# Optimization experiments

Hardware: AMD Instinct MI355X
Metric: run time of the kernel (lower is better)

Reference implementation:

```python
import jax, jax.numpy as jnp
import numpy as np

N_NODES = 100000


def gcn_conv(x, W, b, row, col, ew, n_nodes):
    """PyG GCNConv: add self-loops (weight 1), symmetric normalization,
    out[c] = sum_{(r,c) in E} norm * (x @ W)[r] + b."""
    sl = jnp.arange(n_nodes, dtype=row.dtype)
    row2 = jnp.concatenate([row, sl])
    col2 = jnp.concatenate([col, sl])
    ew2 = jnp.concatenate([ew, jnp.ones((n_nodes,), dtype=ew.dtype)])
    deg = jax.ops.segment_sum(ew2, col2, num_segments=n_nodes)  # [N]
    dinv = jnp.where(deg > 0, jax.lax.rsqrt(jnp.where(deg > 0, deg, 1.0)), 0.0)
    norm = dinv[row2] * ew2 * dinv[col2]                         # [E+N]
    h = x @ W                                                    # [N, out]
    msg = h[row2] * norm[:, None]                                # gather + scale
    out = jax.ops.segment_sum(msg, col2, num_segments=n_nodes)   # scatter-add
    return out + b


def setup_inputs() -> dict:
    key = jax.random.key(0)
    k1, k2, k3, k4, k5 = jax.random.split(key, 5)
    F_IN, HID, C = 512, 16, 40
    E = 3200000
    x = jax.random.normal(k1, (N_NODES, F_IN), dtype=jnp.float32)
    edge_index = jax.random.randint(k2, (2, E), 0, N_NODES, dtype=jnp.int64)
    edge_weight = jax.random.uniform(k3, (E,), dtype=jnp.float32)
    # Glorot-ish init for weights
    W1 = jax.random.normal(k4, (F_IN, HID), dtype=jnp.float32) / np.sqrt(F_IN)
    b1 = jnp.zeros((HID,), dtype=jnp.float32)
    W2 = jax.random.normal(k5, (HID, C), dtype=jnp.float32) / np.sqrt(HID)
    b2 = jnp.zeros((C,), dtype=jnp.float32)
    return {"x": x, "edge_index": edge_index, "edge_weight": edge_weight,
            "W1": W1, "b1": b1, "W2": W2, "b2": b2}


def reference(x, edge_index, edge_weight, W1, b1, W2, b2):
    row, col = edge_index[0], edge_index[1]
    h = jax.nn.relu(gcn_conv(x, W1, b1, row, col, edge_weight, N_NODES))
    # dropout p=0.1 is identity at inference; DFALayer/DFA are identity in forward
    logits = gcn_conv(h, W2, b2, row, col, edge_weight, N_NODES)
    return jax.nn.log_softmax(logits, axis=1)
```

## Files before the change

kernel.cpp:

```cpp
#include <hip/hip_runtime.h>
#include <hip/hip_bf16.h>
#include <math.h>

#define F_IN 512
#define HID  16
#define C_OUT 40

#define BSH    7
#define BNODES 128
#define MAXNB  1024

#define EPB 8192
#define CTH 512

__device__ __forceinline__ unsigned short f2bf(float f) {
    unsigned u = __float_as_uint(f);
    unsigned r = (u + 0x7FFF + ((u >> 16) & 1)) >> 16;
    return (unsigned short)r;
}
__device__ __forceinline__ float bf2f(unsigned short h) {
    return __uint_as_float(((unsigned)h) << 16);
}

__global__ __launch_bounds__(1024) void k_zero(int* __restrict__ g, int n) {
    int t = threadIdx.x;
    if (t < n) g[t] = 0;
}

__global__ __launch_bounds__(CTH) void k_count(const int* __restrict__ col,
                                               int* __restrict__ gcnt,
                                               int E, int NB) {
    __shared__ int lc[MAXNB];
    int t = threadIdx.x;
    for (int i = t; i < NB; i += CTH) lc[i] = 0;
    __syncthreads();
    int base = blockIdx.x * EPB;
#pragma unroll
    for (int i = 0; i < EPB / CTH; ++i) {
        int e = base + t + i * CTH;
        if (e < E) atomicAdd(&lc[col[e] >> BSH], 1);
    }
    __syncthreads();
    for (int i = t; i < NB; i += CTH)
        if (lc[i]) atomicAdd(&gcnt[i], lc[i]);
}

__global__ __launch_bounds__(1024) void k_scan(const int* __restrict__ gcnt,
                                               int* __restrict__ bo,
                                               int* __restrict__ bcur,
                                               int* __restrict__ offs,
                                               int NB, int N, int E) {
    __shared__ int s[1024];
    int t = threadIdx.x;
    int v = (t < NB) ? gcnt[t] : 0;
    s[t] = v;
    __syncthreads();
    for (int off = 1; off < 1024; off <<= 1) {
        int x = (t >= off) ? s[t - off] : 0;
        __syncthreads();
        s[t] += x;
        __syncthreads();
    }
    if (t < NB) { int o = s[t] - v; bo[t] = o; bcur[t] = o; }
    if (t == 0) { bo[NB] = E; offs[N] = E; }
}

__global__ __launch_bounds__(CTH) void k_part(const int* __restrict__ row,
                                              const int* __restrict__ col,
                                              const float* __restrict__ ew,
                                              int* __restrict__ bcur,
                                              int2* __restrict__ st,
                                              int E, int NB) {
    __shared__ int lc[MAXNB];
    __shared__ int lb[MAXNB];
    int t = threadIdx.x;
    for (int i = t; i < NB; i += CTH) lc[i] = 0;
    __syncthreads();
    int base = blockIdx.x * EPB;
#pragma unroll
    for (int i = 0; i < EPB / CTH; ++i) {
        int e = base + t + i * CTH;
        if (e < E) atomicAdd(&lc[col[e] >> BSH], 1);
    }
    __syncthreads();
    for (int i = t; i < NB; i += CTH) {
        int c = lc[i];
        lb[i] = c ? atomicAdd(&bcur[i], c) : 0;
    }
    __syncthreads();
    for (int i = t; i < NB; i += CTH) lc[i] = 0;
    __syncthreads();
#pragma unroll
    for (int i = 0; i < EPB / CTH; ++i) {
        int e = base + t + i * CTH;
        if (e < E) {
            int c = col[e];
            int b = c >> BSH;
            int r = atomicAdd(&lc[b], 1);
            st[lb[b] + r] = make_int2((row[e] << BSH) | (c & (BNODES - 1)),
                                      __float_as_int(ew[e]));
        }
    }
}

__global__ __launch_bounds__(256) void k_sort(const int* __restrict__ bo,
                                              const int2* __restrict__ st,
                                              int2* __restrict__ st2,
                                              int* __restrict__ offs,
                                              float* __restrict__ dinv, int N) {
    __shared__ int cnt[BNODES];
    __shared__ float wsum[BNODES];
    __shared__ int off[BNODES];
    int t = threadIdx.x;
    int b = blockIdx.x;
    if (t < BNODES) { cnt[t] = 0; wsum[t] = 0.0f; }
    __syncthreads();
    int beg = bo[b], end = bo[b + 1];
    for (int e = beg + t; e < end; e += 256) {
        int2 rec = st[e];
        int cl = rec.x & (BNODES - 1);
        atomicAdd(&cnt[cl], 1);
        atomicAdd(&wsum[cl], __int_as_float(rec.y));
    }
    __syncthreads();
    if (t < BNODES) off[t] = cnt[t];
    __syncthreads();
    for (int o = 1; o < BNODES; o <<= 1) {
        int v = (t < BNODES && t >= o) ? off[t - o] : 0;
        __syncthreads();
        if (t < BNODES) off[t] += v;
        __syncthreads();
    }
    if (t < BNODES) {
        int ex = off[t] - cnt[t];
        off[t] = ex;
        int n = b * BNODES + t;
        if (n < N) {
            offs[n] = beg + ex;
            dinv[n] = rsqrtf(1.0f + wsum[t]);
        }
        cnt[t] = 0;
    }
    __syncthreads();
    for (int e = beg + t; e < end; e += 256) {
        int2 rec = st[e];
        int cl = rec.x & (BNODES - 1);
        int r = atomicAdd(&cnt[cl], 1);
        st2[beg + off[cl] + r] = make_int2(rec.x >> BSH, rec.y);
    }
}

#define ROWS_PER_WAVE 16

__global__ __launch_bounds__(256, 1) void k_gemm1(const float* __restrict__ x,
                                                  const float* __restrict__ W,
                                                  const float* __restrict__ dinv,
                                                  unsigned short* __restrict__ hb,
                                                  int N) {
    const int t = threadIdx.x;
    const int lane = t & 63;
    const int wv = blockIdx.x * 4 + (t >> 6);
    const int r0 = wv * ROWS_PER_WAVE;
    if (r0 >= N) return;
    const int rend = (r0 + ROWS_PER_WAVE < N) ? r0 + ROWS_PER_WAVE : N;

    float4 Wa[4][4], Wb[4][4];
    const float4* W4 = (const float4*)W;
#pragma unroll
    for (int q = 0; q < 4; ++q)
#pragma unroll
        for (int j4 = 0; j4 < 4; ++j4) {
            Wa[q][j4] = W4[(4 * lane + q) * 4 + j4];
            Wb[q][j4] = W4[(256 + 4 * lane + q) * 4 + j4];
        }

    const float4* xb4 = (const float4*)x;
    float4 pa = xb4[(size_t)r0 * 128 + lane];
    float4 pb = xb4[(size_t)r0 * 128 + 64 + lane];

    for (int r = r0; r < rend; ++r) {
        float4 ca = pa, cb = pb;
        if (r + 1 < rend) {
            pa = xb4[(size_t)(r + 1) * 128 + lane];
            pb = xb4[(size_t)(r + 1) * 128 + 64 + lane];
        }
        float acc[16];
#pragma unroll
        for (int j = 0; j < 16; ++j) acc[j] = 0.0f;
        const float xs0[4] = {ca.x, ca.y, ca.z, ca.w};
        const float xs1[4] = {cb.x, cb.y, cb.z, cb.w};
#pragma unroll
        for (int q = 0; q < 4; ++q) {
#pragma unroll
            for (int j4 = 0; j4 < 4; ++j4) {
                acc[j4 * 4 + 0] += xs0[q] * Wa[q][j4].x;
                acc[j4 * 4 + 1] += xs0[q] * Wa[q][j4].y;
                acc[j4 * 4 + 2] += xs0[q] * Wa[q][j4].z;
                acc[j4 * 4 + 3] += xs0[q] * Wa[q][j4].w;
            }
        }
#pragma unroll
        for (int q = 0; q < 4; ++q) {
#pragma unroll
            for (int j4 = 0; j4 < 4; ++j4) {
                acc[j4 * 4 + 0] += xs1[q] * Wb[q][j4].x;
                acc[j4 * 4 + 1] += xs1[q] * Wb[q][j4].y;
                acc[j4 * 4 + 2] += xs1[q] * Wb[q][j4].z;
                acc[j4 * 4 + 3] += xs1[q] * Wb[q][j4].w;
            }
        }

        const int b0 = lane & 1;
        float v8[8];
#pragma unroll
        for (int m = 0; m < 8; ++m) {
            float lo = acc[m], hi = acc[m + 8];
            float sent = b0 ? lo : hi;
            float recv = __shfl_xor(sent, 1, 64);
            float keep = b0 ? hi : lo;
            v8[m] = keep + recv;
        }
        const int b1 = (lane >> 1) & 1;
        float v4[4];
#pragma unroll
        for (int m = 0; m < 4; ++m) {
            float lo = v8[m], hi = v8[m + 4];
            float sent = b1 ? lo : hi;
            float recv = __shfl_xor(sent, 2, 64);
            float keep = b1 ? hi : lo;
            v4[m] = keep + recv;
        }
        const int b2 = (lane >> 2) & 1;
        float v2[2];
#pragma unroll
        for (int m = 0; m < 2; ++m) {
            float lo = v4[m], hi = v4[m + 2];
            float sent = b2 ? lo : hi;
            float recv = __shfl_xor(sent, 4, 64);
            float keep = b2 ? hi : lo;
            v2[m] = keep + recv;
        }
        const int b3 = (lane >> 3) & 1;
        float v1;
        {
            float lo = v2[0], hi = v2[1];
            float sent = b3 ? lo : hi;
            float recv = __shfl_xor(sent, 8, 64);
            float keep = b3 ? hi : lo;
            v1 = keep + recv;
        }
        v1 += __shfl_xor(v1, 16, 64);
        v1 += __shfl_xor(v1, 32, 64);

        float d = dinv[r];
        if (lane < 16) {
            int j = ((lane & 1) << 3) | (((lane >> 1) & 1) << 2) |
                    (((lane >> 2) & 1) << 1) | ((lane >> 3) & 1);
            hb[(size_t)r * HID + j] = f2bf(d * v1);
        }
    }
}

__global__ __launch_bounds__(256) void k_agg1(const int* __restrict__ offs,
                                              const int2* __restrict__ st2,
                                              const float* __restrict__ dinv,
                                              const unsigned short* __restrict__ srcb,
                                              const float* __restrict__ bias,
                                              unsigned short* __restrict__ dstb,
                                              int N) {
    int t = threadIdx.x;
    int lane = t & 63, w = t >> 6;
    int n = blockIdx.x * 4 + w;
    if (n >= N) return;
    int q = lane & 3, i = lane >> 2;
    int beg = offs[n], end = offs[n + 1];
    float4 acc = make_float4(0.f, 0.f, 0.f, 0.f);
    for (int e = beg + i; e < end; e += 16) {
        int2 rec = st2[e];
        float wt = __int_as_float(rec.y);
        ushort4 v = ((const ushort4*)(srcb + (size_t)rec.x * HID))[q];
        acc.x += wt * bf2f(v.x);
        acc.y += wt * bf2f(v.y);
        acc.z += wt * bf2f(v.z);
        acc.w += wt * bf2f(v.w);
    }
#pragma unroll
    for (int off = 4; off < 64; off <<= 1) {
        acc.x += __shfl_xor(acc.x, off, 64);
        acc.y += __shfl_xor(acc.y, off, 64);
        acc.z += __shfl_xor(acc.z, off, 64);
        acc.w += __shfl_xor(acc.w, off, 64);
    }
    if (i == 0) {
        float d = dinv[n];
        ushort4 sv = ((const ushort4*)(srcb + (size_t)n * HID))[q];
        float4 bq = ((const float4*)bias)[q];
        float r0 = d * fmaxf(d * (acc.x + bf2f(sv.x)) + bq.x, 0.f);
        float r1 = d * fmaxf(d * (acc.y + bf2f(sv.y)) + bq.y, 0.f);
        float r2 = d * fmaxf(d * (acc.z + bf2f(sv.z)) + bq.z, 0.f);
        float r3 = d * fmaxf(d * (acc.w + bf2f(sv.w)) + bq.w, 0.f);
        ((ushort4*)(dstb + (size_t)n * HID))[q] =
            make_ushort4(f2bf(r0), f2bf(r1), f2bf(r2), f2bf(r3));
    }
}

__global__ __launch_bounds__(256) void k_agg2(const int* __restrict__ offs,
                                              const int2* __restrict__ st2,
                                              const float* __restrict__ dinv,
                                              const unsigned short* __restrict__ srcb,
                                              const float* __restrict__ W2,
                                              const float* __restrict__ b2,
                                              float* __restrict__ out, int N) {
    __shared__ float Ws[HID * C_OUT];
    __shared__ float bs[C_OUT];
    int t = threadIdx.x;
    for (int iw = t; iw < HID * C_OUT; iw += 256) Ws[iw] = W2[iw];
    if (t < C_OUT) bs[t] = b2[t];
    __syncthreads();

    int lane = t & 63, w = t >> 6;
    int n = blockIdx.x * 4 + w;
    if (n >= N) return;
    int q = lane & 3, i = lane >> 2;
    int beg = offs[n], end = offs[n + 1];
    float4 acc = make_float4(0.f, 0.f, 0.f, 0.f);
    for (int e = beg + i; e < end; e += 16) {
        int2 rec = st2[e];
        float wt = __int_as_float(rec.y);
        ushort4 v = ((const ushort4*)(srcb + (size_t)rec.x * HID))[q];
        acc.x += wt * bf2f(v.x);
        acc.y += wt * bf2f(v.y);
        acc.z += wt * bf2f(v.z);
        acc.w += wt * bf2f(v.w);
    }
#pragma unroll
    for (int off = 4; off < 64; off <<= 1) {
        acc.x += __shfl_xor(acc.x, off, 64);
        acc.y += __shfl_xor(acc.y, off, 64);
        acc.z += __shfl_xor(acc.z, off, 64);
        acc.w += __shfl_xor(acc.w, off, 64);
    }
    float d = dinv[n];
    ushort4 sv = ((const ushort4*)(srcb + (size_t)n * HID))[q];
    float gq[4];
    gq[0] = d * (acc.x + bf2f(sv.x));
    gq[1] = d * (acc.y + bf2f(sv.y));
    gq[2] = d * (acc.z + bf2f(sv.z));
    gq[3] = d * (acc.w + bf2f(sv.w));
    float g16[16];
    int base = lane & ~3;
#pragma unroll
    for (int qq = 0; qq < 4; ++qq) {
#pragma unroll
        for (int k = 0; k < 4; ++k)
            g16[qq * 4 + k] = __shfl(gq[k], base + qq, 64);
    }
    float logit = -INFINITY;
    if (lane < C_OUT) {
        float a = bs[lane];
#pragma unroll
        for (int j = 0; j < HID; ++j) a += g16[j] * Ws[j * C_OUT + lane];
        logit = a;
    }
    float m = logit;
#pragma unroll
    for (int off = 32; off > 0; off >>= 1) m = fmaxf(m, __shfl_xor(m, off, 64));
    float ex = (lane < C_OUT) ? __expf(logit - m) : 0.0f;
    float s = ex;
#pragma unroll
    for (int off = 32; off > 0; off >>= 1) s += __shfl_xor(s, off, 64);
    if (lane < C_OUT) out[(size_t)n * C_OUT + lane] = logit - m - __logf(s);
}

extern "C" void kernel_launch(void* const* d_in, const int* in_sizes, int n_in,
                              void* d_out, int out_size, void* d_ws, size_t ws_size,
                              hipStream_t stream) {
    const float* x   = (const float*)d_in[0];
    const int*   ei  = (const int*)d_in[1];
    const float* ew  = (const float*)d_in[2];
    const float* W1  = (const float*)d_in[3];
    const float* b1  = (const float*)d_in[4];
    const float* W2  = (const float*)d_in[5];
    const float* b2  = (const float*)d_in[6];
    float* out = (float*)d_out;

    const int N = in_sizes[0] / F_IN;
    const int E = in_sizes[2];
    const int* row = ei;
    const int* col = ei + E;
    const int NB = (N + BNODES - 1) >> BSH;

    int* wsi = (int*)d_ws;
    size_t o = 0;
    int* gcnt  = wsi + o; o += MAXNB;
    int* bo    = wsi + o; o += MAXNB + 1;
    int* bcur  = wsi + o; o += MAXNB;
    int* offs  = wsi + o; o += (size_t)N + 8;
    float* dinv = (float*)(wsi + o); o += N;
    unsigned short* h1b = (unsigned short*)(wsi + o); o += (size_t)N * HID / 2;
    unsigned short* a1b = (unsigned short*)(wsi + o); o += (size_t)N * HID / 2;
    int2* st   = (int2*)(wsi + o); o += (size_t)E * 2;
    int2* st2  = (int2*)(wsi + o); o += (size_t)E * 2;

    int gC = (E + EPB - 1) / EPB;
    int gW = (N + 3) / 4;
    int gG = (N + 4 * ROWS_PER_WAVE - 1) / (4 * ROWS_PER_WAVE);

    k_zero<<<1, 1024, 0, stream>>>(gcnt, NB);
    k_count<<<gC, CTH, 0, stream>>>(col, gcnt, E, NB);
    k_scan<<<1, 1024, 0, stream>>>(gcnt, bo, bcur, offs, NB, N, E);
    k_part<<<gC, CTH, 0, stream>>>(row, col, ew, bcur, st, E, NB);
    k_sort<<<NB, 256, 0, stream>>>(bo, st, st2, offs, dinv, N);
    k_gemm1<<<gG, 256, 0, stream>>>(x, W1, dinv, h1b, N);
    k_agg1<<<gW, 256, 0, stream>>>(offs, st2, dinv, h1b, b1, a1b, N);
    k_agg2<<<gW, 256, 0, stream>>>(offs, st2, dinv, a1b, W2, b2, out, N);
}
```

Baseline: 594.2 us.

## Drop per-node sort; aggregate bucketed edges via shared-memory atomics per block

Removes the second-level counting sort (k_sort) and CSR offsets. Degree and aggregation now run straight on the bucket-partitioned edge list: each 512-thread block owns a 128-node bucket and scatter-adds weighted neighbor features into a padded shared-memory accumulator, with a one-step software prefetch of the next record. agg2 is restructured so 4 threads per node each compute 10 logits. This saves one full pass over the edge array (read and write of st2) at the cost of LDS float atomics and contention on hot nodes, and it makes accumulation order nondeterministic.

```diff
diff --git a/kernel.cpp b/kernel.cpp
--- a/kernel.cpp
+++ b/kernel.cpp
@@ -12,6 +12,8 @@
 
 #define EPB 8192
 #define CTH 512
+#define ATH 512
+#define APAD 17
 
 __device__ __forceinline__ unsigned short f2bf(float f) {
     unsigned u = __float_as_uint(f);
@@ -48,8 +50,7 @@
 __global__ __launch_bounds__(1024) void k_scan(const int* __restrict__ gcnt,
                                                int* __restrict__ bo,
                                                int* __restrict__ bcur,
-                                               int* __restrict__ offs,
-                                               int NB, int N, int E) {
+                                               int NB, int E) {
     __shared__ int s[1024];
     int t = threadIdx.x;
     int v = (t < NB) ? gcnt[t] : 0;
@@ -62,7 +63,7 @@
         __syncthreads();
     }
     if (t < NB) { int o = s[t] - v; bo[t] = o; bcur[t] = o; }
-    if (t == 0) { bo[NB] = E; offs[N] = E; }
+    if (t == 0) bo[NB] = E;
 }
 
 __global__ __launch_bounds__(CTH) void k_part(const int* __restrict__ row,
@@ -103,50 +104,22 @@
     }
 }
 
-__global__ __launch_bounds__(256) void k_sort(const int* __restrict__ bo,
-                                              const int2* __restrict__ st,
-                                              int2* __restrict__ st2,
-                                              int* __restrict__ offs,
-                                              float* __restrict__ dinv, int N) {
-    __shared__ int cnt[BNODES];
+__global__ __launch_bounds__(ATH) void k_deg(const int* __restrict__ bo,
+                                             const int2* __restrict__ st,
+                                             float* __restrict__ dinv, int N) {
     __shared__ float wsum[BNODES];
-    __shared__ int off[BNODES];
-    int t = threadIdx.x;
-    int b = blockIdx.x;
-    if (t < BNODES) { cnt[t] = 0; wsum[t] = 0.0f; }
+    int t = threadIdx.x, b = blockIdx.x;
+    if (t < BNODES) wsum[t] = 0.0f;
     __syncthreads();
     int beg = bo[b], end = bo[b + 1];
-    for (int e = beg + t; e < end; e += 256) {
+    for (int e = beg + t; e < end; e += ATH) {
         int2 rec = st[e];
-        int cl = rec.x & (BNODES - 1);
-        atomicAdd(&cnt[cl], 1);
-        atomicAdd(&wsum[cl], __int_as_float(rec.y));
-    }
-    __syncthreads();
-    if (t < BNODES) off[t] = cnt[t];
-    __syncthreads();
-    for (int o = 1; o < BNODES; o <<= 1) {
-        int v = (t < BNODES && t >= o) ? off[t - o] : 0;
-        __syncthreads();
-        if (t < BNODES) off[t] += v;
-        __syncthreads();
-    }
+        atomicAdd(&wsum[rec.x & (BNODES - 1)], __int_as_float(rec.y));
+    }
+    __syncthreads();
     if (t < BNODES) {
-        int ex = off[t] - cnt[t];
-        off[t] = ex;
         int n = b * BNODES + t;
-        if (n < N) {
-            offs[n] = beg + ex;
-            dinv[n] = rsqrtf(1.0f + wsum[t]);
-        }
-        cnt[t] = 0;
-    }
-    __syncthreads();
-    for (int e = beg + t; e < end; e += 256) {
-        int2 rec = st[e];
-        int cl = rec.x & (BNODES - 1);
-        int r = atomicAdd(&cnt[cl], 1);
-        st2[beg + off[cl] + r] = make_int2(rec.x >> BSH, rec.y);
+        if (n < N) dinv[n] = rsqrtf(1.0f + wsum[t]);
     }
 }
 
@@ -261,115 +234,145 @@
     }
 }
 
-__global__ __launch_bounds__(256) void k_agg1(const int* __restrict__ offs,
-                                              const int2* __restrict__ st2,
+__global__ __launch_bounds__(ATH) void k_agg1(const int* __restrict__ bo,
+                                              const int2* __restrict__ st,
                                               const float* __restrict__ dinv,
                                               const unsigned short* __restrict__ srcb,
                                               const float* __restrict__ bias,
                                               unsigned short* __restrict__ dstb,
                                               int N) {
-    int t = threadIdx.x;
-    int lane = t & 63, w = t >> 6;
-    int n = blockIdx.x * 4 + w;
-    if (n >= N) return;
-    int q = lane & 3, i = lane >> 2;
-    int beg = offs[n], end = offs[n + 1];
-    float4 acc = make_float4(0.f, 0.f, 0.f, 0.f);
-    for (int e = beg + i; e < end; e += 16) {
-        int2 rec = st2[e];
-        float wt = __int_as_float(rec.y);
-        ushort4 v = ((const ushort4*)(srcb + (size_t)rec.x * HID))[q];
-        acc.x += wt * bf2f(v.x);
-        acc.y += wt * bf2f(v.y);
-        acc.z += wt * bf2f(v.z);
-        acc.w += wt * bf2f(v.w);
-    }
-#pragma unroll
-    for (int off = 4; off < 64; off <<= 1) {
-        acc.x += __shfl_xor(acc.x, off, 64);
-        acc.y += __shfl_xor(acc.y, off, 64);
-        acc.z += __shfl_xor(acc.z, off, 64);
-        acc.w += __shfl_xor(acc.w, off, 64);
-    }
-    if (i == 0) {
+    __shared__ float acc[BNODES * APAD];
+    int t = threadIdx.x, b = blockIdx.x;
+    for (int i = t; i < BNODES * APAD; i += ATH) acc[i] = 0.0f;
+    __syncthreads();
+
+    int beg = bo[b], end = bo[b + 1];
+    const int q = t & 3;
+    int e0 = beg + (t >> 2);
+    int2 r0 = make_int2(0, 0);
+    float4 v0 = make_float4(0.f, 0.f, 0.f, 0.f);
+    if (e0 < end) {
+        r0 = st[e0];
+        ushort4 u = ((const ushort4*)(srcb + (size_t)(r0.x >> BSH) * HID))[q];
+        v0 = make_float4(bf2f(u.x), bf2f(u.y), bf2f(u.z), bf2f(u.w));
+    }
+    while (e0 < end) {
+        int e1 = e0 + (ATH / 4);
+        int2 r1 = r0;
+        float4 v1 = v0;
+        if (e1 < end) {
+            r1 = st[e1];
+            ushort4 u = ((const ushort4*)(srcb + (size_t)(r1.x >> BSH) * HID))[q];
+            v1 = make_float4(bf2f(u.x), bf2f(u.y), bf2f(u.z), bf2f(u.w));
+        }
+        float wt = __int_as_float(r0.y);
+        float* a = &acc[(r0.x & (BNODES - 1)) * APAD + q * 4];
+        atomicAdd(a + 0, wt * v0.x);
+        atomicAdd(a + 1, wt * v0.y);
+        atomicAdd(a + 2, wt * v0.z);
+        atomicAdd(a + 3, wt * v0.w);
+        e0 = e1; r0 = r1; v0 = v1;
+    }
+    __syncthreads();
+
+    int nl = t >> 2;
+    int n = b * BNODES + nl;
+    if (n < N) {
         float d = dinv[n];
         ushort4 sv = ((const ushort4*)(srcb + (size_t)n * HID))[q];
         float4 bq = ((const float4*)bias)[q];
-        float r0 = d * fmaxf(d * (acc.x + bf2f(sv.x)) + bq.x, 0.f);
-        float r1 = d * fmaxf(d * (acc.y + bf2f(sv.y)) + bq.y, 0.f);
-        float r2 = d * fmaxf(d * (acc.z + bf2f(sv.z)) + bq.z, 0.f);
-        float r3 = d * fmaxf(d * (acc.w + bf2f(sv.w)) + bq.w, 0.f);
+        const float* a = &acc[nl * APAD + q * 4];
+        float o0 = d * fmaxf(d * (a[0] + bf2f(sv.x)) + bq.x, 0.f);
+        float o1 = d * fmaxf(d * (a[1] + bf2f(sv.y)) + bq.y, 0.f);
+        float o2 = d * fmaxf(d * (a[2] + bf2f(sv.z)) + bq.z, 0.f);
+        float o3 = d * fmaxf(d * (a[3] + bf2f(sv.w)) + bq.w, 0.f);
         ((ushort4*)(dstb + (size_t)n * HID))[q] =
-            make_ushort4(f2bf(r0), f2bf(r1), f2bf(r2), f2bf(r3));
-    }
-}
-
-__global__ __launch_bounds__(256) void k_agg2(const int* __restrict__ offs,
-                                              const int2* __restrict__ st2,
+            make_ushort4(f2bf(o0), f2bf(o1), f2bf(o2), f2bf(o3));
+    }
+}
+
+__global__ __launch_bounds__(ATH) void k_agg2(const int* __restrict__ bo,
+                                              const int2* __restrict__ st,
                                               const float* __restrict__ dinv,
                                               const unsigned short* __restrict__ srcb,
                                               const float* __restrict__ W2,
                                               const float* __restrict__ b2,
                                               float* __restrict__ out, int N) {
+    __shared__ float acc[BNODES * APAD];
     __shared__ float Ws[HID * C_OUT];
     __shared__ float bs[C_OUT];
-    int t = threadIdx.x;
-    for (int iw = t; iw < HID * C_OUT; iw += 256) Ws[iw] = W2[iw];
+    int t = threadIdx.x, b = blockIdx.x;
+    for (int i = t; i < BNODES * APAD; i += ATH) acc[i] = 0.0f;
+    for (int i = t; i < HID * C_OUT; i += ATH) Ws[i] = W2[i];
     if (t < C_OUT) bs[t] = b2[t];
     __syncthreads();
 
-    int lane = t & 63, w = t >> 6;
-    int n = blockIdx.x * 4 + w;
+    int beg = bo[b], end = bo[b + 1];
+    const int q = t & 3;
+    int e0 = beg + (t >> 2);
+    int2 r0 = make_int2(0, 0);
+    float4 v0 = make_float4(0.f, 0.f, 0.f, 0.f);
+    if (e0 < end) {
+        r0 = st[e0];
+        ushort4 u = ((const ushort4*)(srcb + (size_t)(r0.x >> BSH) * HID))[q];
+        v0 = make_float4(bf2f(u.x), bf2f(u.y), bf2f(u.z), bf2f(u.w));
+    }
+    while (e0 < end) {
+        int e1 = e0 + (ATH / 4);
+        int2 r1 = r0;
+        float4 v1 = v0;
+        if (e1 < end) {
+            r1 = st[e1];
+            ushort4 u = ((const ushort4*)(srcb + (size_t)(r1.x >> BSH) * HID))[q];
+            v1 = make_float4(bf2f(u.x), bf2f(u.y), bf2f(u.z), bf2f(u.w));
+        }
+        float wt = __int_as_float(r0.y);
+        float* a = &acc[(r0.x & (BNODES - 1)) * APAD + q * 4];
+        atomicAdd(a + 0, wt * v0.x);
+        atomicAdd(a + 1, wt * v0.y);
+        atomicAdd(a + 2, wt * v0.z);
+        atomicAdd(a + 3, wt * v0.w);
+        e0 = e1; r0 = r1; v0 = v1;
+    }
+    __syncthreads();
+
+    int nl = t >> 2;
+    int n = b * BNODES + nl;
     if (n >= N) return;
-    int q = lane & 3, i = lane >> 2;
-    int beg = offs[n], end = offs[n + 1];
-    float4 acc = make_float4(0.f, 0.f, 0.f, 0.f);
-    for (int e = beg + i; e < end; e += 16) {
-        int2 rec = st2[e];
-        float wt = __int_as_float(rec.y);
-        ushort4 v = ((const ushort4*)(srcb + (size_t)rec.x * HID))[q];
-        acc.x += wt * bf2f(v.x);
-        acc.y += wt * bf2f(v.y);
-        acc.z += wt * bf2f(v.z);
-        acc.w += wt * bf2f(v.w);
-    }
-#pragma unroll
-    for (int off = 4; off < 64; off <<= 1) {
-        acc.x += __shfl_xor(acc.x, off, 64);
-        acc.y += __shfl_xor(acc.y, off, 64);
-        acc.z += __shfl_xor(acc.z, off, 64);
-        acc.w += __shfl_xor(acc.w, off, 64);
-    }
     float d = dinv[n];
-    ushort4 sv = ((const ushort4*)(srcb + (size_t)n * HID))[q];
-    float gq[4];
-    gq[0] = d * (acc.x + bf2f(sv.x));
-    gq[1] = d * (acc.y + bf2f(sv.y));
-    gq[2] = d * (acc.z + bf2f(sv.z));
-    gq[3] = d * (acc.w + bf2f(sv.w));
     float g16[16];
-    int base = lane & ~3;
-#pragma unroll
-    for (int qq = 0; qq < 4; ++qq) {
-#pragma unroll
-        for (int k = 0; k < 4; ++k)
-            g16[qq * 4 + k] = __shfl(gq[k], base + qq, 64);
-    }
-    float logit = -INFINITY;
-    if (lane < C_OUT) {
-        float a = bs[lane];
-#pragma unroll
-        for (int j = 0; j < HID; ++j) a += g16[j] * Ws[j * C_OUT + lane];
-        logit = a;
-    }
-    float m = logit;
-#pragma unroll
-    for (int off = 32; off > 0; off >>= 1) m = fmaxf(m, __shfl_xor(m, off, 64));
-    float ex = (lane < C_OUT) ? __expf(logit - m) : 0.0f;
-    float s = ex;
-#pragma unroll
-    for (int off = 32; off > 0; off >>= 1) s += __shfl_xor(s, off, 64);
-    if (lane < C_OUT) out[(size_t)n * C_OUT + lane] = logit - m - __logf(s);
+    const ushort4* sp = (const ushort4*)(srcb + (size_t)n * HID);
+#pragma unroll
+    for (int p = 0; p < 4; ++p) {
+        ushort4 sv = sp[p];
+        const float* a = &acc[nl * APAD + p * 4];
+        g16[p * 4 + 0] = d * (a[0] + bf2f(sv.x));
+        g16[p * 4 + 1] = d * (a[1] + bf2f(sv.y));
+        g16[p * 4 + 2] = d * (a[2] + bf2f(sv.z));
+        g16[p * 4 + 3] = d * (a[3] + bf2f(sv.w));
+    }
+    const int cb = q * 10;
+    float lg[10];
+    float m = -INFINITY;
+#pragma unroll
+    for (int c = 0; c < 10; ++c) {
+        float a = bs[cb + c];
+#pragma unroll
+        for (int j = 0; j < HID; ++j) a += g16[j] * Ws[j * C_OUT + cb + c];
+        lg[c] = a;
+        m = fmaxf(m, a);
+    }
+    m = fmaxf(m, __shfl_xor(m, 1, 64));
+    m = fmaxf(m, __shfl_xor(m, 2, 64));
+    float s = 0.0f;
+#pragma unroll
+    for (int c = 0; c < 10; ++c) s += __expf(lg[c] - m);
+    s += __shfl_xor(s, 1, 64);
+    s += __shfl_xor(s, 2, 64);
+    float ls = __logf(s);
+    float* op = out + (size_t)n * C_OUT + cb;
+#pragma unroll
+    for (int c = 0; c < 10; ++c) op[c] = lg[c] - m - ls;
 }
 
 extern "C" void kernel_launch(void* const* d_in, const int* in_sizes, int n_in,
@@ -395,23 +398,20 @@
     int* gcnt  = wsi + o; o += MAXNB;
     int* bo    = wsi + o; o += MAXNB + 1;
     int* bcur  = wsi + o; o += MAXNB;
-    int* offs  = wsi + o; o += (size_t)N + 8;
     float* dinv = (float*)(wsi + o); o += N;
     unsigned short* h1b = (unsigned short*)(wsi + o); o += (size_t)N * HID / 2;
     unsigned short* a1b = (unsigned short*)(wsi + o); o += (size_t)N * HID / 2;
     int2* st   = (int2*)(wsi + o); o += (size_t)E * 2;
-    int2* st2  = (int2*)(wsi + o); o += (size_t)E * 2;
 
     int gC = (E + EPB - 1) / EPB;
-    int gW = (N + 3) / 4;
     int gG = (N + 4 * ROWS_PER_WAVE - 1) / (4 * ROWS_PER_WAVE);
 
     k_zero<<<1, 1024, 0, stream>>>(gcnt, NB);
     k_count<<<gC, CTH, 0, stream>>>(col, gcnt, E, NB);
-    k_scan<<<1, 1024, 0, stream>>>(gcnt, bo, bcur, offs, NB, N, E);
+    k_scan<<<1, 1024, 0, stream>>>(gcnt, bo, bcur, NB, E);
     k_part<<<gC, CTH, 0, stream>>>(row, col, ew, bcur, st, E, NB);
-    k_sort<<<NB, 256, 0, stream>>>(bo, st, st2, offs, dinv, N);
+    k_deg<<<NB, ATH, 0, stream>>>(bo, st, dinv, N);
     k_gemm1<<<gG, 256, 0, stream>>>(x, W1, dinv, h1b, N);
-    k_agg1<<<gW, 256, 0, stream>>>(offs, st2, dinv, h1b, b1, a1b, N);
-    k_agg2<<<gW, 256, 0, stream>>>(offs, st2, dinv, a1b, W2, b2, out, N);
-}
+    k_agg1<<<NB, ATH, 0, stream>>>(bo, st, dinv, h1b, b1, a1b, N);
+    k_agg2<<<NB, ATH, 0, stream>>>(bo, st, dinv, a1b, W2, b2, out, N);
+}
```

Result: slower. 1.128 ms (+89.8%).
